# Kernel tuning notes

Hardware: AMD Instinct MI355X
Metric: run time of the kernel (lower is better)

Reference implementation:

```python
import jax, jax.numpy as jnp
import numpy as np

N_NODES = 100000
N_EDGES = 1600000
DIN = 128
DOUT = 128
N_SUP = 2


def setup_inputs() -> dict:
    key = jax.random.key(0)
    k = jax.random.split(key, 6)
    x = jax.random.normal(k[0], (N_NODES, DIN), dtype=jnp.float32)
    w = jax.random.normal(k[1], (N_SUP, DIN, DOUT), dtype=jnp.float32) * (1.0 / np.sqrt(DIN))
    bias = jax.random.normal(k[2], (DOUT,), dtype=jnp.float32) * 0.01
    sup_vals = jax.random.uniform(k[3], (N_SUP, N_EDGES), dtype=jnp.float32)
    sup_rows = jax.random.randint(k[4], (N_SUP, N_EDGES), 0, N_NODES, dtype=jnp.int32)
    sup_cols = jax.random.randint(k[5], (N_SUP, N_EDGES), 0, N_NODES, dtype=jnp.int32)
    return {"x": x, "w": w, "bias": bias, "sup_vals": sup_vals,
            "sup_rows": sup_rows, "sup_cols": sup_cols}


def _spmm(vals, rows, cols, dense):
    # COO sparse [N,N] @ dense [N,D] -> [N,D]
    gathered = vals[:, None] * dense[cols]        # [E, D]
    return jax.ops.segment_sum(gathered, rows, num_segments=N_NODES)


def reference(x, w, bias, sup_vals, sup_rows, sup_cols):
    # pre_sup_i = x @ w_i for each support: [S, N, Dout]
    pre = jnp.einsum('nd,sdo->sno', x, w)
    # SpMM per support, vmapped over the support axis, then summed
    supports = jax.vmap(_spmm)(sup_vals, sup_rows, sup_cols, pre)  # [S, N, Dout]
    out = supports.sum(axis=0) + bias
    return jax.nn.relu(out)
```

## Files before the change

### kernel.cpp

```cpp
#include <hip/hip_runtime.h>

#define N_NODES 100000
#define N_EDGES 1600000
#define DIN 128
#define DOUT 128
#define N_SUP 2
#define E_TOT (N_SUP * N_EDGES)

#define BIN_ROWS 128
#define BSHIFT 7
#define NBINS ((N_NODES + BIN_ROWS - 1) / BIN_ROWS)

#define SC_EPT 16
#define SC_BLOCK 256
#define SC_CHUNK (SC_EPT * SC_BLOCK)
#define NBLK_SC ((E_TOT + SC_CHUNK - 1) / SC_CHUNK)

#define GEMM_ROWS 128
#define LDK 136

typedef float        f32x2 __attribute__((ext_vector_type(2)));
typedef float        f32x4 __attribute__((ext_vector_type(4)));
typedef unsigned int u32;
typedef u32          u32x2 __attribute__((ext_vector_type(2)));
typedef u32          u32x4 __attribute__((ext_vector_type(4)));
typedef short        bf16x8 __attribute__((ext_vector_type(8)));

static __device__ __forceinline__ u32 pack_bf16x2(float lo, float hi) {
    u32 ul = __float_as_uint(lo);
    u32 uh = __float_as_uint(hi);
    ul = (ul + 0x7FFFu + ((ul >> 16) & 1u)) >> 16;
    uh = ((uh + 0x7FFFu + ((uh >> 16) & 1u)) >> 16) << 16;
    return ul | uh;
}

__global__ __launch_bounds__(256) void xconv_kernel(const float* __restrict__ x,
                                                    u32* __restrict__ xb) {
    const int idx = blockIdx.x * 256 + threadIdx.x;
    const int total = N_NODES * 64 / 4;
    if (idx < total) {
        const float* p = x + (size_t)idx * 8;
        const f32x4 a = __builtin_nontemporal_load((const f32x4*)p);
        const f32x4 b = __builtin_nontemporal_load((const f32x4*)(p + 4));
        u32x4 o;
        o.x = pack_bf16x2(a.x, a.y);
        o.y = pack_bf16x2(a.z, a.w);
        o.z = pack_bf16x2(b.x, b.y);
        o.w = pack_bf16x2(b.z, b.w);
        __builtin_nontemporal_store(o, (u32x4*)(xb + (size_t)idx * 4));
    }
}

__global__ __launch_bounds__(256) void wconv_kernel(const float* __restrict__ w,
                                                    u32* __restrict__ wTb) {
    const int s = blockIdx.x;
    const int n = threadIdx.x >> 1;
    const int kh = (threadIdx.x & 1) * 64;
    const float* wp = w + (size_t)s * DIN * DOUT + n;
    u32 o[32];
    #pragma unroll
    for (int j = 0; j < 32; j++) {
        const float lo = wp[(size_t)(kh + 2 * j) * DOUT];
        const float hi = wp[(size_t)(kh + 2 * j + 1) * DOUT];
        o[j] = pack_bf16x2(lo, hi);
    }
    u32* op = wTb + ((size_t)s * 128 + n) * 64 + kh / 2;
    #pragma unroll
    for (int j = 0; j < 8; j++)
        *(u32x4*)(op + j * 4) = *(u32x4*)&o[j * 4];
}

__global__ __launch_bounds__(256) void mfma_gemm_kernel(const u32* __restrict__ xb,
                                                        const u32* __restrict__ wTb,
                                                        u32* __restrict__ pre) {
    __shared__ alignas(16) unsigned short stage[2][GEMM_ROWS][LDK];
    float (*epi)[129] = (float (*)[129])(void*)stage;

    const int s = blockIdx.y;
    const int row0 = blockIdx.x * GEMM_ROWS;
    const int t = threadIdx.x;
    const int lane = t & 63;
    const int wv = t >> 6;

    {
        const int r = t >> 1;
        const int half = t & 1;
        const int gr = row0 + r;
        u32* dst = (u32*)&stage[0][r][half * 64];
        if (gr < N_NODES) {
            const u32* p = xb + (size_t)gr * 64 + half * 32;
            #pragma unroll
            for (int j = 0; j < 8; j++)
                *(u32x4*)(dst + j * 4) = *(const u32x4*)(p + j * 4);
        } else {
            #pragma unroll
            for (int j = 0; j < 8; j++)
                *(u32x4*)(dst + j * 4) = (u32x4){0, 0, 0, 0};
        }
        const u32* wp = wTb + ((size_t)s * 128 + r) * 64 + half * 32;
        u32* wdst = (u32*)&stage[1][r][half * 64];
        #pragma unroll
        for (int j = 0; j < 8; j++)
            *(u32x4*)(wdst + j * 4) = *(const u32x4*)(wp + j * 4);
    }
    __syncthreads();

    const int q = lane >> 4;
    const int ml = lane & 15;
    const int m0 = wv * 32;

    f32x4 acc[2][8];
    #pragma unroll
    for (int mt = 0; mt < 2; mt++)
        #pragma unroll
        for (int nt = 0; nt < 8; nt++) acc[mt][nt] = (f32x4){0.f, 0.f, 0.f, 0.f};

    #pragma unroll
    for (int kt = 0; kt < 4; kt++) {
        const int k0 = kt * 32 + q * 8;
        const bf16x8 a0 = *(const bf16x8*)&stage[0][m0 + ml][k0];
        const bf16x8 a1 = *(const bf16x8*)&stage[0][m0 + 16 + ml][k0];
        #pragma unroll
        for (int nt = 0; nt < 8; nt++) {
            const bf16x8 b = *(const bf16x8*)&stage[1][nt * 16 + ml][k0];
            acc[0][nt] = __builtin_amdgcn_mfma_f32_16x16x32_bf16(a0, b, acc[0][nt], 0, 0, 0);
            acc[1][nt] = __builtin_amdgcn_mfma_f32_16x16x32_bf16(a1, b, acc[1][nt], 0, 0, 0);
        }
    }
    __syncthreads();

    #pragma unroll
    for (int mt = 0; mt < 2; mt++)
        #pragma unroll
        for (int nt = 0; nt < 8; nt++)
            #pragma unroll
            for (int r = 0; r < 4; r++)
                epi[m0 + mt * 16 + q * 4 + r][nt * 16 + ml] = acc[mt][nt][r];
    __syncthreads();

    {
        const int row = t >> 1;
        const int half = t & 1;
        const int gr = row0 + row;
        if (gr < N_NODES) {
            u32 ov[32];
            #pragma unroll
            for (int j = 0; j < 32; j++)
                ov[j] = pack_bf16x2(epi[row][half * 64 + 2 * j],
                                    epi[row][half * 64 + 2 * j + 1]);
            u32* op = pre + ((size_t)s * N_NODES + gr) * 64 + half * 32;
            #pragma unroll
            for (int j = 0; j < 8; j++)
                __builtin_nontemporal_store(*(u32x4*)&ov[j * 4], (u32x4*)(op + j * 4));
        }
    }
}

__global__ __launch_bounds__(256) void binhist_kernel(const int* __restrict__ rows,
                                                      int* __restrict__ bin_cnt) {
    __shared__ int h[NBINS];
    const int t = threadIdx.x;
    for (int i = t; i < NBINS; i += 256) h[i] = 0;
    __syncthreads();
    const int base = blockIdx.x * SC_CHUNK;
    #pragma unroll
    for (int j = 0; j < SC_EPT; j++) {
        const int i = base + j * 256 + t;
        if (i < E_TOT) atomicAdd(&h[__builtin_nontemporal_load(rows + i) >> BSHIFT], 1);
    }
    __syncthreads();
    for (int i = t; i < NBINS; i += 256)
        if (h[i]) atomicAdd(&bin_cnt[i], h[i]);
}

__global__ __launch_bounds__(1024) void binscan_kernel(const int* __restrict__ bin_cnt,
                                                       int* __restrict__ bin_base,
                                                       int* __restrict__ bin_cursor) {
    __shared__ int s[1024];
    const int t = threadIdx.x;
    const int v = (t < NBINS) ? bin_cnt[t] : 0;
    s[t] = v;
    __syncthreads();
    #pragma unroll
    for (int off = 1; off < 1024; off <<= 1) {
        const int u = (t >= off) ? s[t - off] : 0;
        __syncthreads();
        s[t] += u;
        __syncthreads();
    }
    if (t < NBINS) {
        const int ex = s[t] - v;
        bin_base[t] = ex;
        bin_cursor[t] = ex;
    }
    if (t == 0) bin_base[NBINS] = E_TOT;
}

__global__ __launch_bounds__(256) void binscatter_kernel(const int* __restrict__ rows,
                                                         const int* __restrict__ cols,
                                                         const float* __restrict__ vals,
                                                         int* __restrict__ bin_cursor,
                                                         u32x2* __restrict__ edata) {
    __shared__ int lcnt[NBINS];
    __shared__ int lbase[NBINS];
    const int t = threadIdx.x;
    for (int i = t; i < NBINS; i += 256) lcnt[i] = 0;
    __syncthreads();

    const int base = blockIdx.x * SC_CHUNK;
    int bin[SC_EPT], lpos[SC_EPT];
    u32x2 pay[SC_EPT];
    #pragma unroll
    for (int j = 0; j < SC_EPT; j++) {
        const int i = base + j * 256 + t;
        if (i < E_TOT) {
            const int r = __builtin_nontemporal_load(rows + i);
            const int c = __builtin_nontemporal_load(cols + i);
            const float v = __builtin_nontemporal_load(vals + i);
            const int b = r >> BSHIFT;
            bin[j] = b;
            lpos[j] = atomicAdd(&lcnt[b], 1);
            pay[j].x = (u32)(c + ((i >= N_EDGES) ? N_NODES : 0)) |
                       ((u32)(r & (BIN_ROWS - 1)) << 18);
            pay[j].y = __float_as_uint(v);
        } else {
            bin[j] = -1;
        }
    }
    __syncthreads();
    for (int b = t; b < NBINS; b += 256) {
        const int c = lcnt[b];
        if (c) lbase[b] = atomicAdd(&bin_cursor[b], c);
    }
    __syncthreads();
    #pragma unroll
    for (int j = 0; j < SC_EPT; j++) {
        if (bin[j] >= 0) edata[lbase[bin[j]] + lpos[j]] = pay[j];
    }
}

__global__ __launch_bounds__(256) void binsort_kernel(const u32x2* __restrict__ edata,
                                                      u32x2* __restrict__ edata2,
                                                      const int* __restrict__ bin_base,
                                                      int* __restrict__ row_start) {
    __shared__ int rcnt[BIN_ROWS];
    __shared__ int rscan[BIN_ROWS];
    const int t = threadIdx.x;
    const int b = blockIdx.x;
    const int beg = bin_base[b];
    const int end = bin_base[b + 1];

    if (t < BIN_ROWS) rcnt[t] = 0;
    __syncthreads();
    for (int e = beg + t; e < end; e += 256)
        atomicAdd(&rcnt[edata[e].x >> 18], 1);
    __syncthreads();

    const int v = (t < BIN_ROWS) ? rcnt[t] : 0;
    if (t < BIN_ROWS) rscan[t] = v;
    __syncthreads();
    #pragma unroll
    for (int off = 1; off < BIN_ROWS; off <<= 1) {
        const int u = (t < BIN_ROWS && t >= off) ? rscan[t - off] : 0;
        __syncthreads();
        if (t < BIN_ROWS) rscan[t] += u;
        __syncthreads();
    }
    if (t < BIN_ROWS) {
        const int ex = rscan[t] - v;
        rcnt[t] = ex;
        const int row = b * BIN_ROWS + t;
        if (row < N_NODES) row_start[row] = beg + ex;
    }
    __syncthreads();
    for (int e = beg + t; e < end; e += 256) {
        const u32x2 d = edata[e];
        const int pos = beg + atomicAdd(&rcnt[d.x >> 18], 1);
        u32x2 o;
        o.x = d.x & 0x3FFFFu;
        o.y = d.y;
        edata2[pos] = o;
    }
    if (b == NBINS - 1 && t == 0) row_start[N_NODES] = E_TOT;
}

__global__ __launch_bounds__(256, 8) void gather_kernel(const u32* __restrict__ pre,
                                                        const u32x2* __restrict__ edata2,
                                                        const int* __restrict__ row_start,
                                                        const float* __restrict__ bias,
                                                        float* __restrict__ out) {
    const int lane = threadIdx.x & 63;
    const int wid = threadIdx.x >> 6;
    const int row = blockIdx.x * 4 + wid;
    if (row >= N_NODES) return;

    const int beg = row_start[row];
    const int end = row_start[row + 1];

    float ax = 0.f, ay = 0.f;
    int e = beg;

    for (; e + 8 <= end; e += 8) {
        u32x2 d[8];
        #pragma unroll
        for (int j = 0; j < 8; j++)
            d[j] = __builtin_nontemporal_load(edata2 + e + j);
        u32 u[8];
        #pragma unroll
        for (int j = 0; j < 8; j++)
            u[j] = pre[(u32)((d[j].x << 6) + (u32)lane)];
        #pragma unroll
        for (int j = 0; j < 8; j++) {
            const float v = __uint_as_float(d[j].y);
            ax = fmaf(v, __uint_as_float(u[j] << 16), ax);
            ay = fmaf(v, __uint_as_float(u[j] & 0xFFFF0000u), ay);
        }
    }
    for (; e + 4 <= end; e += 4) {
        u32x2 d[4];
        #pragma unroll
        for (int j = 0; j < 4; j++)
            d[j] = __builtin_nontemporal_load(edata2 + e + j);
        u32 u[4];
        #pragma unroll
        for (int j = 0; j < 4; j++)
            u[j] = pre[(u32)((d[j].x << 6) + (u32)lane)];
        #pragma unroll
        for (int j = 0; j < 4; j++) {
            const float v = __uint_as_float(d[j].y);
            ax = fmaf(v, __uint_as_float(u[j] << 16), ax);
            ay = fmaf(v, __uint_as_float(u[j] & 0xFFFF0000u), ay);
        }
    }
    for (; e < end; e++) {
        const u32x2 d = __builtin_nontemporal_load(edata2 + e);
        const u32 u = pre[(u32)((d.x << 6) + (u32)lane)];
        const float v = __uint_as_float(d.y);
        ax = fmaf(v, __uint_as_float(u << 16), ax);
        ay = fmaf(v, __uint_as_float(u & 0xFFFF0000u), ay);
    }

    const float2 b = *(const float2*)(bias + lane * 2);
    f32x2 r;
    r.x = fmaxf(ax + b.x, 0.f);
    r.y = fmaxf(ay + b.y, 0.f);
    __builtin_nontemporal_store(r, (f32x2*)(out + (size_t)row * DOUT + lane * 2));
}

extern "C" void kernel_launch(void* const* d_in, const int* in_sizes, int n_in,
                              void* d_out, int out_size, void* d_ws, size_t ws_size,
                              hipStream_t stream) {
    (void)in_sizes; (void)n_in; (void)out_size; (void)ws_size;
    const float* x        = (const float*)d_in[0];
    const float* w        = (const float*)d_in[1];
    const float* bias     = (const float*)d_in[2];
    const float* sup_vals = (const float*)d_in[3];
    const int*   sup_rows = (const int*)d_in[4];
    const int*   sup_cols = (const int*)d_in[5];
    float* out = (float*)d_out;

    char* ws = (char*)d_ws;
    u32*   pre       = (u32*)ws;
    u32x2* edata     = (u32x2*)(ws + (size_t)N_SUP * N_NODES * 64 * 4);
    u32x2* edata2    = (u32x2*)((char*)edata + (size_t)E_TOT * 8);
    u32*   xb        = (u32*)edata2;
    int*   bin_cnt   = (int*)((char*)edata2 + (size_t)E_TOT * 8);
    int*   bin_base  = bin_cnt + NBINS;
    int*   bin_cursor= bin_base + NBINS + 1;
    int*   row_start = bin_cursor + NBINS;
    u32*   wTb       = (u32*)(row_start + N_NODES + 1);

    xconv_kernel<<<(N_NODES * 64 / 4 + 255) / 256, 256, 0, stream>>>(x, xb);
    wconv_kernel<<<N_SUP, 256, 0, stream>>>(w, wTb);
    {
        dim3 grid((N_NODES + GEMM_ROWS - 1) / GEMM_ROWS, N_SUP);
        mfma_gemm_kernel<<<grid, 256, 0, stream>>>(xb, wTb, pre);
    }
    (void)hipMemsetAsync(bin_cnt, 0, NBINS * sizeof(int), stream);
    binhist_kernel<<<NBLK_SC, 256, 0, stream>>>(sup_rows, bin_cnt);
    binscan_kernel<<<1, 1024, 0, stream>>>(bin_cnt, bin_base, bin_cursor);
    binscatter_kernel<<<NBLK_SC, 256, 0, stream>>>(sup_rows, sup_cols, sup_vals,
                                                   bin_cursor, edata);
    binsort_kernel<<<NBINS, 256, 0, stream>>>(edata, edata2, bin_base, row_start);
    gather_kernel<<<(N_NODES + 3) / 4, 256, 0, stream>>>(pre, edata2, row_start, bias, out);
}
```

Before: 446.1 us.

## Reorder to aggregate-then-transform: SpMM on x first, then single fused GEMM

Measured after the change: 498.3 us. +11.7%, slower.

```diff
diff --git a/kernel.cpp b/kernel.cpp
--- a/kernel.cpp
+++ b/kernel.cpp
@@ -18,6 +18,9 @@
 
 #define GEMM_ROWS 128
 #define LDK 136
+
+#define COL_MASK 0x1FFFFu
+#define SUP_BIT  0x20000u
 
 typedef float        f32x2 __attribute__((ext_vector_type(2)));
 typedef float        f32x4 __attribute__((ext_vector_type(4)));
@@ -64,96 +67,10 @@
         const float hi = wp[(size_t)(kh + 2 * j + 1) * DOUT];
         o[j] = pack_bf16x2(lo, hi);
     }
-    u32* op = wTb + ((size_t)s * 128 + n) * 64 + kh / 2;
+    u32* op = wTb + (size_t)n * 128 + s * 64 + kh / 2;
     #pragma unroll
     for (int j = 0; j < 8; j++)
         *(u32x4*)(op + j * 4) = *(u32x4*)&o[j * 4];
-}
-
-__global__ __launch_bounds__(256) void mfma_gemm_kernel(const u32* __restrict__ xb,
-                                                        const u32* __restrict__ wTb,
-                                                        u32* __restrict__ pre) {
-    __shared__ alignas(16) unsigned short stage[2][GEMM_ROWS][LDK];
-    float (*epi)[129] = (float (*)[129])(void*)stage;
-
-    const int s = blockIdx.y;
-    const int row0 = blockIdx.x * GEMM_ROWS;
-    const int t = threadIdx.x;
-    const int lane = t & 63;
-    const int wv = t >> 6;
-
-    {
-        const int r = t >> 1;
-        const int half = t & 1;
-        const int gr = row0 + r;
-        u32* dst = (u32*)&stage[0][r][half * 64];
-        if (gr < N_NODES) {
-            const u32* p = xb + (size_t)gr * 64 + half * 32;
-            #pragma unroll
-            for (int j = 0; j < 8; j++)
-                *(u32x4*)(dst + j * 4) = *(const u32x4*)(p + j * 4);
-        } else {
-            #pragma unroll
-            for (int j = 0; j < 8; j++)
-                *(u32x4*)(dst + j * 4) = (u32x4){0, 0, 0, 0};
-        }
-        const u32* wp = wTb + ((size_t)s * 128 + r) * 64 + half * 32;
-        u32* wdst = (u32*)&stage[1][r][half * 64];
-        #pragma unroll
-        for (int j = 0; j < 8; j++)
-            *(u32x4*)(wdst + j * 4) = *(const u32x4*)(wp + j * 4);
-    }
-    __syncthreads();
-
-    const int q = lane >> 4;
-    const int ml = lane & 15;
-    const int m0 = wv * 32;
-
-    f32x4 acc[2][8];
-    #pragma unroll
-    for (int mt = 0; mt < 2; mt++)
-        #pragma unroll
-        for (int nt = 0; nt < 8; nt++) acc[mt][nt] = (f32x4){0.f, 0.f, 0.f, 0.f};
-
-    #pragma unroll
-    for (int kt = 0; kt < 4; kt++) {
-        const int k0 = kt * 32 + q * 8;
-        const bf16x8 a0 = *(const bf16x8*)&stage[0][m0 + ml][k0];
-        const bf16x8 a1 = *(const bf16x8*)&stage[0][m0 + 16 + ml][k0];
-        #pragma unroll
-        for (int nt = 0; nt < 8; nt++) {
-            const bf16x8 b = *(const bf16x8*)&stage[1][nt * 16 + ml][k0];
-            acc[0][nt] = __builtin_amdgcn_mfma_f32_16x16x32_bf16(a0, b, acc[0][nt], 0, 0, 0);
-            acc[1][nt] = __builtin_amdgcn_mfma_f32_16x16x32_bf16(a1, b, acc[1][nt], 0, 0, 0);
-        }
-    }
-    __syncthreads();
-
-    #pragma unroll
-    for (int mt = 0; mt < 2; mt++)
-        #pragma unroll
-        for (int nt = 0; nt < 8; nt++)
-            #pragma unroll
-            for (int r = 0; r < 4; r++)
-                epi[m0 + mt * 16 + q * 4 + r][nt * 16 + ml] = acc[mt][nt][r];
-    __syncthreads();
-
-    {
-        const int row = t >> 1;
-        const int half = t & 1;
-        const int gr = row0 + row;
-        if (gr < N_NODES) {
-            u32 ov[32];
-            #pragma unroll
-            for (int j = 0; j < 32; j++)
-                ov[j] = pack_bf16x2(epi[row][half * 64 + 2 * j],
-                                    epi[row][half * 64 + 2 * j + 1]);
-            u32* op = pre + ((size_t)s * N_NODES + gr) * 64 + half * 32;
-            #pragma unroll
-            for (int j = 0; j < 8; j++)
-                __builtin_nontemporal_store(*(u32x4*)&ov[j * 4], (u32x4*)(op + j * 4));
-        }
-    }
 }
 
 __global__ __launch_bounds__(256) void binhist_kernel(const int* __restrict__ rows,
@@ -220,7 +137,7 @@
             const int b = r >> BSHIFT;
             bin[j] = b;
             lpos[j] = atomicAdd(&lcnt[b], 1);
-            pay[j].x = (u32)(c + ((i >= N_EDGES) ? N_NODES : 0)) |
+            pay[j].x = (u32)c | ((i >= N_EDGES) ? SUP_BIT : 0u) |
                        ((u32)(r & (BIN_ROWS - 1)) << 18);
             pay[j].y = __float_as_uint(v);
         } else {
@@ -284,11 +201,10 @@
     if (b == NBINS - 1 && t == 0) row_start[N_NODES] = E_TOT;
 }
 
-__global__ __launch_bounds__(256, 8) void gather_kernel(const u32* __restrict__ pre,
+__global__ __launch_bounds__(256, 8) void gather_kernel(const u32* __restrict__ xb,
                                                         const u32x2* __restrict__ edata2,
                                                         const int* __restrict__ row_start,
-                                                        const float* __restrict__ bias,
-                                                        float* __restrict__ out) {
+                                                        u32* __restrict__ Y) {
     const int lane = threadIdx.x & 63;
     const int wid = threadIdx.x >> 6;
     const int row = blockIdx.x * 4 + wid;
@@ -297,7 +213,7 @@
     const int beg = row_start[row];
     const int end = row_start[row + 1];
 
-    float ax = 0.f, ay = 0.f;
+    float a0x = 0.f, a0y = 0.f, a1x = 0.f, a1y = 0.f;
     int e = beg;
 
     for (; e + 8 <= end; e += 8) {
@@ -308,12 +224,19 @@
         u32 u[8];
         #pragma unroll
         for (int j = 0; j < 8; j++)
-            u[j] = pre[(u32)((d[j].x << 6) + (u32)lane)];
+            u[j] = xb[(u32)(((d[j].x & COL_MASK) << 6) + (u32)lane)];
         #pragma unroll
         for (int j = 0; j < 8; j++) {
             const float v = __uint_as_float(d[j].y);
-            ax = fmaf(v, __uint_as_float(u[j] << 16), ax);
-            ay = fmaf(v, __uint_as_float(u[j] & 0xFFFF0000u), ay);
+            const bool s1 = (d[j].x & SUP_BIT) != 0u;
+            const float v0 = s1 ? 0.f : v;
+            const float v1 = s1 ? v : 0.f;
+            const float lo = __uint_as_float(u[j] << 16);
+            const float hi = __uint_as_float(u[j] & 0xFFFF0000u);
+            a0x = fmaf(v0, lo, a0x);
+            a0y = fmaf(v0, hi, a0y);
+            a1x = fmaf(v1, lo, a1x);
+            a1y = fmaf(v1, hi, a1y);
         }
     }
     for (; e + 4 <= end; e += 4) {
@@ -324,27 +247,156 @@
         u32 u[4];
         #pragma unroll
         for (int j = 0; j < 4; j++)
-            u[j] = pre[(u32)((d[j].x << 6) + (u32)lane)];
+            u[j] = xb[(u32)(((d[j].x & COL_MASK) << 6) + (u32)lane)];
         #pragma unroll
         for (int j = 0; j < 4; j++) {
             const float v = __uint_as_float(d[j].y);
-            ax = fmaf(v, __uint_as_float(u[j] << 16), ax);
-            ay = fmaf(v, __uint_as_float(u[j] & 0xFFFF0000u), ay);
+            const bool s1 = (d[j].x & SUP_BIT) != 0u;
+            const float v0 = s1 ? 0.f : v;
+            const float v1 = s1 ? v : 0.f;
+            const float lo = __uint_as_float(u[j] << 16);
+            const float hi = __uint_as_float(u[j] & 0xFFFF0000u);
+            a0x = fmaf(v0, lo, a0x);
+            a0y = fmaf(v0, hi, a0y);
+            a1x = fmaf(v1, lo, a1x);
+            a1y = fmaf(v1, hi, a1y);
         }
     }
     for (; e < end; e++) {
         const u32x2 d = __builtin_nontemporal_load(edata2 + e);
-        const u32 u = pre[(u32)((d.x << 6) + (u32)lane)];
+        const u32 u = xb[(u32)(((d.x & COL_MASK) << 6) + (u32)lane)];
         const float v = __uint_as_float(d.y);
-        ax = fmaf(v, __uint_as_float(u << 16), ax);
-        ay = fmaf(v, __uint_as_float(u & 0xFFFF0000u), ay);
-    }
-
-    const float2 b = *(const float2*)(bias + lane * 2);
-    f32x2 r;
-    r.x = fmaxf(ax + b.x, 0.f);
-    r.y = fmaxf(ay + b.y, 0.f);
-    __builtin_nontemporal_store(r, (f32x2*)(out + (size_t)row * DOUT + lane * 2));
+        const bool s1 = (d.x & SUP_BIT) != 0u;
+        const float v0 = s1 ? 0.f : v;
+        const float v1 = s1 ? v : 0.f;
+        const float lo = __uint_as_float(u << 16);
+        const float hi = __uint_as_float(u & 0xFFFF0000u);
+        a0x = fmaf(v0, lo, a0x);
+        a0y = fmaf(v0, hi, a0y);
+        a1x = fmaf(v1, lo, a1x);
+        a1y = fmaf(v1, hi, a1y);
+    }
+
+    u32* yp = Y + (size_t)row * 128;
+    __builtin_nontemporal_store(pack_bf16x2(a0x, a0y), yp + lane);
+    __builtin_nontemporal_store(pack_bf16x2(a1x, a1y), yp + 64 + lane);
+}
+
+__global__ __launch_bounds__(256) void mfma_gemm_kernel(const u32* __restrict__ Y,
+                                                        const u32* __restrict__ wTb,
+                                                        const float* __restrict__ bias,
+                                                        float* __restrict__ out) {
+    __shared__ alignas(16) unsigned short stage[2][GEMM_ROWS][LDK];
+    float (*epi)[129] = (float (*)[129])(void*)stage;
+
+    const int row0 = blockIdx.x * GEMM_ROWS;
+    const int t = threadIdx.x;
+    const int lane = t & 63;
+    const int wv = t >> 6;
+
+    const int q = lane >> 4;
+    const int ml = lane & 15;
+    const int m0 = wv * 32;
+
+    f32x4 acc[2][8];
+    #pragma unroll
+    for (int mt = 0; mt < 2; mt++)
+        #pragma unroll
+        for (int nt = 0; nt < 8; nt++) acc[mt][nt] = (f32x4){0.f, 0.f, 0.f, 0.f};
+
+    const int r = t >> 1;
+    const int half = t & 1;
+    const int gr = row0 + r;
+
+    {
+        u32* dst = (u32*)&stage[0][r][half * 64];
+        if (gr < N_NODES) {
+            const u32* p = Y + (size_t)gr * 128 + half * 32;
+            #pragma unroll
+            for (int j = 0; j < 8; j++)
+                *(u32x4*)(dst + j * 4) = *(const u32x4*)(p + j * 4);
+        } else {
+            #pragma unroll
+            for (int j = 0; j < 8; j++)
+                *(u32x4*)(dst + j * 4) = (u32x4){0, 0, 0, 0};
+        }
+        const u32* wp = wTb + (size_t)r * 128 + half * 32;
+        u32* wdst = (u32*)&stage[1][r][half * 64];
+        #pragma unroll
+        for (int j = 0; j < 8; j++)
+            *(u32x4*)(wdst + j * 4) = *(const u32x4*)(wp + j * 4);
+    }
+    __syncthreads();
+    #pragma unroll
+    for (int kt = 0; kt < 4; kt++) {
+        const int k0 = kt * 32 + q * 8;
+        const bf16x8 a0 = *(const bf16x8*)&stage[0][m0 + ml][k0];
+        const bf16x8 a1 = *(const bf16x8*)&stage[0][m0 + 16 + ml][k0];
+        #pragma unroll
+        for (int nt = 0; nt < 8; nt++) {
+            const bf16x8 b = *(const bf16x8*)&stage[1][nt * 16 + ml][k0];
+            acc[0][nt] = __builtin_amdgcn_mfma_f32_16x16x32_bf16(a0, b, acc[0][nt], 0, 0, 0);
+            acc[1][nt] = __builtin_amdgcn_mfma_f32_16x16x32_bf16(a1, b, acc[1][nt], 0, 0, 0);
+        }
+    }
+    __syncthreads();
+
+    {
+        u32* dst = (u32*)&stage[0][r][half * 64];
+        if (gr < N_NODES) {
+            const u32* p = Y + (size_t)gr * 128 + 64 + half * 32;
+            #pragma unroll
+            for (int j = 0; j < 8; j++)
+                *(u32x4*)(dst + j * 4) = *(const u32x4*)(p + j * 4);
+        } else {
+            #pragma unroll
+            for (int j = 0; j < 8; j++)
+                *(u32x4*)(dst + j * 4) = (u32x4){0, 0, 0, 0};
+        }
+        const u32* wp = wTb + (size_t)r * 128 + 64 + half * 32;
+        u32* wdst = (u32*)&stage[1][r][half * 64];
+        #pragma unroll
+        for (int j = 0; j < 8; j++)
+            *(u32x4*)(wdst + j * 4) = *(const u32x4*)(wp + j * 4);
+    }
+    __syncthreads();
+    #pragma unroll
+    for (int kt = 0; kt < 4; kt++) {
+        const int k0 = kt * 32 + q * 8;
+        const bf16x8 a0 = *(const bf16x8*)&stage[0][m0 + ml][k0];
+        const bf16x8 a1 = *(const bf16x8*)&stage[0][m0 + 16 + ml][k0];
+        #pragma unroll
+        for (int nt = 0; nt < 8; nt++) {
+            const bf16x8 b = *(const bf16x8*)&stage[1][nt * 16 + ml][k0];
+            acc[0][nt] = __builtin_amdgcn_mfma_f32_16x16x32_bf16(a0, b, acc[0][nt], 0, 0, 0);
+            acc[1][nt] = __builtin_amdgcn_mfma_f32_16x16x32_bf16(a1, b, acc[1][nt], 0, 0, 0);
+        }
+    }
+    __syncthreads();
+
+    #pragma unroll
+    for (int mt = 0; mt < 2; mt++)
+        #pragma unroll
+        for (int nt = 0; nt < 8; nt++)
+            #pragma unroll
+            for (int rr = 0; rr < 4; rr++)
+                epi[m0 + mt * 16 + q * 4 + rr][nt * 16 + ml] = acc[mt][nt][rr];
+    __syncthreads();
+
+    if (gr < N_NODES) {
+        float* op = out + (size_t)gr * DOUT + half * 64;
+        const float* bp = bias + half * 64;
+        #pragma unroll
+        for (int j = 0; j < 16; j++) {
+            const f32x4 bv = *(const f32x4*)(bp + j * 4);
+            f32x4 v = *(const f32x4*)&epi[r][half * 64 + j * 4];
+            v.x = fmaxf(v.x + bv.x, 0.f);
+            v.y = fmaxf(v.y + bv.y, 0.f);
+            v.z = fmaxf(v.z + bv.z, 0.f);
+            v.w = fmaxf(v.w + bv.w, 0.f);
+            __builtin_nontemporal_store(v, (f32x4*)(op + j * 4));
+        }
+    }
 }
 
 extern "C" void kernel_launch(void* const* d_in, const int* in_sizes, int n_in,
@@ -360,11 +412,12 @@
     float* out = (float*)d_out;
 
     char* ws = (char*)d_ws;
-    u32*   pre       = (u32*)ws;
-    u32x2* edata     = (u32x2*)(ws + (size_t)N_SUP * N_NODES * 64 * 4);
-    u32x2* edata2    = (u32x2*)((char*)edata + (size_t)E_TOT * 8);
-    u32*   xb        = (u32*)edata2;
-    int*   bin_cnt   = (int*)((char*)edata2 + (size_t)E_TOT * 8);
+    u32*   xb     = (u32*)ws;
+    u32x2* edata2 = (u32x2*)(ws + (size_t)N_NODES * 64 * 4);
+    char*  regC   = (char*)edata2 + (size_t)E_TOT * 8;
+    u32x2* edata  = (u32x2*)regC;
+    u32*   Y      = (u32*)regC;
+    int*   bin_cnt   = (int*)(regC + (size_t)N_NODES * 128 * 4);
     int*   bin_base  = bin_cnt + NBINS;
     int*   bin_cursor= bin_base + NBINS + 1;
     int*   row_start = bin_cursor + NBINS;
@@ -372,15 +425,12 @@
 
     xconv_kernel<<<(N_NODES * 64 / 4 + 255) / 256, 256, 0, stream>>>(x, xb);
     wconv_kernel<<<N_SUP, 256, 0, stream>>>(w, wTb);
-    {
-        dim3 grid((N_NODES + GEMM_ROWS - 1) / GEMM_ROWS, N_SUP);
-        mfma_gemm_kernel<<<grid, 256, 0, stream>>>(xb, wTb, pre);
-    }
     (void)hipMemsetAsync(bin_cnt, 0, NBINS * sizeof(int), stream);
     binhist_kernel<<<NBLK_SC, 256, 0, stream>>>(sup_rows, bin_cnt);
     binscan_kernel<<<1, 1024, 0, stream>>>(bin_cnt, bin_base, bin_cursor);
     binscatter_kernel<<<NBLK_SC, 256, 0, stream>>>(sup_rows, sup_cols, sup_vals,
                                                    bin_cursor, edata);
     binsort_kernel<<<NBINS, 256, 0, stream>>>(edata, edata2, bin_base, row_start);
-    gather_kernel<<<(N_NODES + 3) / 4, 256, 0, stream>>>(pre, edata2, row_start, bias, out);
-}
+    gather_kernel<<<(N_NODES + 3) / 4, 256, 0, stream>>>(xb, edata2, row_start, Y);
+    mfma_gemm_kernel<<<(N_NODES + GEMM_ROWS - 1) / GEMM_ROWS, 256, 0, stream>>>(Y, wTb, bias, out);
+}
```

## Fuse x bf16 conversion into GEMM load and software-pipeline gather edge loads

Applied to the files above, without the earlier changes.

Measured after the change: 432.3 us. 1.03x faster.

```diff
diff --git a/kernel.cpp b/kernel.cpp
--- a/kernel.cpp
+++ b/kernel.cpp
@@ -32,23 +32,6 @@
     ul = (ul + 0x7FFFu + ((ul >> 16) & 1u)) >> 16;
     uh = ((uh + 0x7FFFu + ((uh >> 16) & 1u)) >> 16) << 16;
     return ul | uh;
-}
-
-__global__ __launch_bounds__(256) void xconv_kernel(const float* __restrict__ x,
-                                                    u32* __restrict__ xb) {
-    const int idx = blockIdx.x * 256 + threadIdx.x;
-    const int total = N_NODES * 64 / 4;
-    if (idx < total) {
-        const float* p = x + (size_t)idx * 8;
-        const f32x4 a = __builtin_nontemporal_load((const f32x4*)p);
-        const f32x4 b = __builtin_nontemporal_load((const f32x4*)(p + 4));
-        u32x4 o;
-        o.x = pack_bf16x2(a.x, a.y);
-        o.y = pack_bf16x2(a.z, a.w);
-        o.z = pack_bf16x2(b.x, b.y);
-        o.w = pack_bf16x2(b.z, b.w);
-        __builtin_nontemporal_store(o, (u32x4*)(xb + (size_t)idx * 4));
-    }
 }
 
 __global__ __launch_bounds__(256) void wconv_kernel(const float* __restrict__ w,
@@ -70,7 +53,7 @@
         *(u32x4*)(op + j * 4) = *(u32x4*)&o[j * 4];
 }
 
-__global__ __launch_bounds__(256) void mfma_gemm_kernel(const u32* __restrict__ xb,
+__global__ __launch_bounds__(256) void mfma_gemm_kernel(const float* __restrict__ x,
                                                         const u32* __restrict__ wTb,
                                                         u32* __restrict__ pre) {
     __shared__ alignas(16) unsigned short stage[2][GEMM_ROWS][LDK];
@@ -87,16 +70,22 @@
         const int half = t & 1;
         const int gr = row0 + r;
         u32* dst = (u32*)&stage[0][r][half * 64];
+        u32 o[32];
         if (gr < N_NODES) {
-            const u32* p = xb + (size_t)gr * 64 + half * 32;
-            #pragma unroll
-            for (int j = 0; j < 8; j++)
-                *(u32x4*)(dst + j * 4) = *(const u32x4*)(p + j * 4);
+            const float* p = x + (size_t)gr * DIN + half * 64;
+            #pragma unroll
+            for (int j = 0; j < 16; j++) {
+                const f32x4 a = *(const f32x4*)(p + j * 4);
+                o[2 * j]     = pack_bf16x2(a.x, a.y);
+                o[2 * j + 1] = pack_bf16x2(a.z, a.w);
+            }
         } else {
             #pragma unroll
-            for (int j = 0; j < 8; j++)
-                *(u32x4*)(dst + j * 4) = (u32x4){0, 0, 0, 0};
-        }
+            for (int j = 0; j < 32; j++) o[j] = 0;
+        }
+        #pragma unroll
+        for (int j = 0; j < 8; j++)
+            *(u32x4*)(dst + j * 4) = *(u32x4*)&o[j * 4];
         const u32* wp = wTb + ((size_t)s * 128 + r) * 64 + half * 32;
         u32* wdst = (u32*)&stage[1][r][half * 64];
         #pragma unroll
@@ -284,7 +273,7 @@
     if (b == NBINS - 1 && t == 0) row_start[N_NODES] = E_TOT;
 }
 
-__global__ __launch_bounds__(256, 8) void gather_kernel(const u32* __restrict__ pre,
+__global__ __launch_bounds__(256, 6) void gather_kernel(const u32* __restrict__ pre,
                                                         const u32x2* __restrict__ edata2,
                                                         const int* __restrict__ row_start,
                                                         const float* __restrict__ bias,
@@ -300,20 +289,34 @@
     float ax = 0.f, ay = 0.f;
     int e = beg;
 
-    for (; e + 8 <= end; e += 8) {
+    if (e + 8 <= end) {
         u32x2 d[8];
         #pragma unroll
         for (int j = 0; j < 8; j++)
             d[j] = __builtin_nontemporal_load(edata2 + e + j);
-        u32 u[8];
-        #pragma unroll
-        for (int j = 0; j < 8; j++)
-            u[j] = pre[(u32)((d[j].x << 6) + (u32)lane)];
-        #pragma unroll
-        for (int j = 0; j < 8; j++) {
-            const float v = __uint_as_float(d[j].y);
-            ax = fmaf(v, __uint_as_float(u[j] << 16), ax);
-            ay = fmaf(v, __uint_as_float(u[j] & 0xFFFF0000u), ay);
+        for (;;) {
+            u32 u[8];
+            #pragma unroll
+            for (int j = 0; j < 8; j++)
+                u[j] = pre[(u32)((d[j].x << 6) + (u32)lane)];
+            const int en = e + 8;
+            const bool more = (en + 8 <= end);
+            u32x2 dn[8];
+            if (more) {
+                #pragma unroll
+                for (int j = 0; j < 8; j++)
+                    dn[j] = __builtin_nontemporal_load(edata2 + en + j);
+            }
+            #pragma unroll
+            for (int j = 0; j < 8; j++) {
+                const float v = __uint_as_float(d[j].y);
+                ax = fmaf(v, __uint_as_float(u[j] << 16), ax);
+                ay = fmaf(v, __uint_as_float(u[j] & 0xFFFF0000u), ay);
+            }
+            e = en;
+            if (!more) break;
+            #pragma unroll
+            for (int j = 0; j < 8; j++) d[j] = dn[j];
         }
     }
     for (; e + 4 <= end; e += 4) {
@@ -363,18 +366,16 @@
     u32*   pre       = (u32*)ws;
     u32x2* edata     = (u32x2*)(ws + (size_t)N_SUP * N_NODES * 64 * 4);
     u32x2* edata2    = (u32x2*)((char*)edata + (size_t)E_TOT * 8);
-    u32*   xb        = (u32*)edata2;
     int*   bin_cnt   = (int*)((char*)edata2 + (size_t)E_TOT * 8);
     int*   bin_base  = bin_cnt + NBINS;
     int*   bin_cursor= bin_base + NBINS + 1;
     int*   row_start = bin_cursor + NBINS;
     u32*   wTb       = (u32*)(row_start + N_NODES + 1);
 
-    xconv_kernel<<<(N_NODES * 64 / 4 + 255) / 256, 256, 0, stream>>>(x, xb);
     wconv_kernel<<<N_SUP, 256, 0, stream>>>(w, wTb);
     {
         dim3 grid((N_NODES + GEMM_ROWS - 1) / GEMM_ROWS, N_SUP);
-        mfma_gemm_kernel<<<grid, 256, 0, stream>>>(xb, wTb, pre);
+        mfma_gemm_kernel<<<grid, 256, 0, stream>>>(x, wTb, pre);
     }
     (void)hipMemsetAsync(bin_cnt, 0, NBINS * sizeof(int), stream);
     binhist_kernel<<<NBLK_SC, 256, 0, stream>>>(sup_rows, bin_cnt);
```
